# Optimization experiments

Hardware: AMD Instinct MI355X
Metric: run time of the kernel (lower is better)

The kernel has to match this reference:

```python
import jax, jax.numpy as jnp
import numpy as np

B, N, D, H = 8, 1024, 768, 12
HD = D // H  # head_dim = 64


def setup_inputs() -> dict:
    key = jax.random.key(0)
    ks = jax.random.split(key, 7)
    s = 1.0 / np.sqrt(D)  # xavier-ish scale for weights
    return {
        "x1": jax.random.normal(ks[0], (B, N, D), dtype=jnp.float32),
        "x2": jax.random.normal(ks[1], (B, N, D), dtype=jnp.float32),
        "Wq": jax.random.normal(ks[2], (D, D), dtype=jnp.float32) * s,
        "Wk": jax.random.normal(ks[3], (D, D), dtype=jnp.float32) * s,
        "Wv": jax.random.normal(ks[4], (D, D), dtype=jnp.float32) * s,
        "Wo": jax.random.normal(ks[5], (D, D), dtype=jnp.float32) * s,
        "bo": jnp.zeros((D,), dtype=jnp.float32),
    }


def _heads(x):
    # (B, N, D) -> (B, H, N, HD)
    return x.reshape(B, -1, H, HD).transpose(0, 2, 1, 3)


def reference(x1, x2, Wq, Wk, Wv, Wo, bo):
    scale = 1.0 / jnp.sqrt(jnp.asarray(HD, x1.dtype))
    q1 = _heads(x1 @ Wq.T)               # (B,H,N,HD)
    k1 = _heads(x1 @ Wk.T)
    v1 = _heads(x1 @ Wv.T)
    k2 = _heads(x2 @ Wk.T)
    v2 = _heads(x2 @ Wv.T)
    kc = jnp.concatenate([k1, k2], axis=2)   # (B,H,2N,HD)
    vc = jnp.concatenate([v1, v2], axis=2)
    attn = jnp.einsum('bhnd,bhmd->bhnm', q1, kc) * scale  # (B,H,N,2N)
    attn = jax.nn.softmax(attn, axis=-1)
    out = jnp.einsum('bhnm,bhmd->bhnd', attn, vc)          # (B,H,N,HD)
    out = out.transpose(0, 2, 1, 3).reshape(B, N, D)
    return out @ Wo.T + bo
```

## Files before the change

### kernel.cpp

```cpp
#include <hip/hip_runtime.h>


typedef __bf16 bf16x8 __attribute__((ext_vector_type(8)));
typedef float  f32x4  __attribute__((ext_vector_type(4)));
typedef unsigned int u32x4 __attribute__((ext_vector_type(4)));
typedef short  s16x4  __attribute__((ext_vector_type(4)));

__device__ __forceinline__ unsigned short bf16bits(float f) {
    return __builtin_bit_cast(unsigned short, (__bf16)f);
}
__device__ __forceinline__ unsigned pk2(float a, float b) {
    return (unsigned)bf16bits(a) | ((unsigned)bf16bits(b) << 16);
}
__device__ __forceinline__ bf16x8 asbf(u32x4 v) {
    return __builtin_bit_cast(bf16x8, v);
}
__device__ __forceinline__ float fexp2(float x) {
#if __has_builtin(__builtin_amdgcn_exp2f)
    return __builtin_amdgcn_exp2f(x);
#else
    return exp2f(x);
#endif
}
__device__ __forceinline__ float frcp(float x) {
#if __has_builtin(__builtin_amdgcn_rcpf)
    return __builtin_amdgcn_rcpf(x);
#else
    return 1.0f / x;
#endif
}

#define MFMA32(a, b, c) __builtin_amdgcn_mfma_f32_16x16x32_bf16((a), (b), (c), 0, 0, 0)

__global__ __launch_bounds__(256) void convert_all(
    const float* __restrict__ x1, const float* __restrict__ x2,
    const float* __restrict__ Wq, const float* __restrict__ Wk,
    const float* __restrict__ Wv, const float* __restrict__ Wo,
    unsigned short* __restrict__ x1b, unsigned short* __restrict__ x2b,
    unsigned short* __restrict__ Wcat, unsigned short* __restrict__ Wob)
{
    const float* src; unsigned short* dst; int n4;
    switch (blockIdx.y) {
        case 0:  src = x1; dst = x1b;            n4 = 1572864; break;
        case 1:  src = x2; dst = x2b;            n4 = 1572864; break;
        case 2:  src = Wq; dst = Wcat;           n4 = 147456;  break;
        case 3:  src = Wk; dst = Wcat +  589824; n4 = 147456;  break;
        case 4:  src = Wv; dst = Wcat + 1179648; n4 = 147456;  break;
        default: src = Wo; dst = Wob;            n4 = 147456;  break;
    }
    int i = blockIdx.x * 256 + threadIdx.x;
    if (i >= n4) return;
    float4 v = ((const float4*)src)[i];
    unsigned* o32 = (unsigned*)(dst + (size_t)i * 4);
    o32[0] = pk2(v.x, v.y);
    o32[1] = pk2(v.z, v.w);
}

template<int MODE>
__global__ __launch_bounds__(256) void gemm_qkv(
    const unsigned short* __restrict__ A1, const unsigned short* __restrict__ A2,
    const unsigned short* __restrict__ Wcat,
    unsigned short* __restrict__ dQ, unsigned short* __restrict__ dK,
    unsigned short* __restrict__ dV)
{
    __shared__ u32x4 smA[2048];
    __shared__ u32x4 smB[2048];

    const int tid  = threadIdx.x;
    const int lane = tid & 63;
    const int l15  = lane & 15;
    const int g    = lane >> 4;
    const int wid  = tid >> 6;
    const int rb   = blockIdx.x;
    const int jb   = blockIdx.y;
    const int wr   = (wid >> 1) * 64;
    const int wc   = (wid & 1) * 64;

    const bool br2 = (jb >= 18);
    const unsigned short* A  = br2 ? A2 : A1;
    const unsigned short* Bw = br2 ? (Wcat + 589824) : Wcat;
    const int jcol = br2 ? (jb - 18) : jb;

    f32x4 acc[4][4] = {};

#define GSTAGE(KT, BO)                                                               \
    {                                                                                \
        int kt_ = (KT);                                                              \
        _Pragma("unroll")                                                            \
        for (int c_ = 0; c_ < 4; ++c_) {                                             \
            int i_   = (wid + c_ * 4) * 64 + lane;                                   \
            int row_ = i_ >> 3;                                                      \
            int gs_  = (i_ & 7) ^ (row_ & 7);                                        \
            const unsigned short* sa = A +                                           \
                (size_t)(rb * 128 + row_) * 768 + kt_ * 64 + gs_ * 8;                \
            __builtin_amdgcn_global_load_lds(                                        \
                (const __attribute__((address_space(1))) void*)sa,                   \
                (__attribute__((address_space(3))) void*)(smA + (BO) + (wid + c_ * 4) * 64), \
                16, 0, 0);                                                           \
            const unsigned short* sb = Bw +                                          \
                (size_t)(jcol * 128 + row_) * 768 + kt_ * 64 + gs_ * 8;              \
            __builtin_amdgcn_global_load_lds(                                        \
                (const __attribute__((address_space(1))) void*)sb,                   \
                (__attribute__((address_space(3))) void*)(smB + (BO) + (wid + c_ * 4) * 64), \
                16, 0, 0);                                                           \
        }                                                                            \
    }

    GSTAGE(0, 0)

    for (int kt = 0; kt < 12; ++kt) {
        __builtin_amdgcn_s_barrier();
        if (kt < 11) {
            GSTAGE(kt + 1, ((kt + 1) & 1) << 10)
            asm volatile("s_waitcnt vmcnt(8)" ::: "memory");
        } else {
            asm volatile("s_waitcnt vmcnt(0)" ::: "memory");
        }
        __builtin_amdgcn_s_barrier();
        __builtin_amdgcn_sched_barrier(0);

        const u32x4* bA = smA + ((kt & 1) << 10);
        const u32x4* bB = smB + ((kt & 1) << 10);

#pragma unroll
        for (int kk = 0; kk < 2; ++kk) {
            bf16x8 af[4], bfr[4];
#pragma unroll
            for (int m = 0; m < 4; ++m) {
                int row = wr + m * 16 + l15;
                af[m] = asbf(bA[row * 8 + ((kk * 4 + g) ^ (row & 7))]);
            }
#pragma unroll
            for (int n = 0; n < 4; ++n) {
                int row = wc + n * 16 + l15;
                bfr[n] = asbf(bB[row * 8 + ((kk * 4 + g) ^ (row & 7))]);
            }
#pragma unroll
            for (int m = 0; m < 4; ++m)
#pragma unroll
                for (int n = 0; n < 4; ++n)
                    acc[m][n] = MFMA32(af[m], bfr[n], acc[m][n]);
        }
    }
#undef GSTAGE

    const int rloc = wr + g * 4;
    const int cloc = wc + l15;
    const int seg  = jcol / 6;
#pragma unroll
    for (int m = 0; m < 4; ++m) {
#pragma unroll
        for (int n = 0; n < 4; ++n) {
            int r0 = rb * 128 + rloc + m * 16;
            int c  = jcol * 128 + cloc + n * 16;
            int b = r0 >> 10, nn = r0 & 1023;
            int cl = c - seg * 768;
            int h = cl >> 6, hd = cl & 63;
            int segq = br2 ? seg + 3 : seg;
            if (segq == 0) {
#pragma unroll
                for (int reg = 0; reg < 4; ++reg)
                    dQ[((size_t)(b * 12 + h) * 1024 + nn + reg) * 64 + hd] =
                        bf16bits(acc[m][n][reg] * 0.18033688f);
            } else if (segq == 1 || segq == 3) {
                size_t koff = (segq == 3) ? 1024 : 0;
#pragma unroll
                for (int reg = 0; reg < 4; ++reg)
                    dK[((size_t)(b * 12 + h) * 2048 + koff + nn + reg) * 64 + hd] =
                        bf16bits(acc[m][n][reg]);
            } else {
                size_t koff = (segq == 4) ? 1024 : 0;
                uint2 w;
                w.x = pk2(acc[m][n][0], acc[m][n][1]);
                w.y = pk2(acc[m][n][2], acc[m][n][3]);
                *(uint2*)(dV + ((size_t)(b * 12 + h) * 64 + hd) * 2048 +
                          koff + nn) = w;
            }
        }
    }
}

__global__ __launch_bounds__(256) void gemm_out(
    const unsigned short* __restrict__ A, const unsigned short* __restrict__ Bw,
    float* __restrict__ dO, const float* __restrict__ bias)
{
    __shared__ u32x4 smA[2048];
    __shared__ u32x4 smB[2048];

    const int tid  = threadIdx.x;
    const int lane = tid & 63;
    const int l15  = lane & 15;
    const int g    = lane >> 4;
    const int wid  = tid >> 6;
    const int rb   = blockIdx.x;
    const int jb   = blockIdx.y;
    const int wr   = (wid >> 1) * 64;
    const int wc   = (wid & 1) * 64;

    f32x4 acc[4][4] = {};

#define GSTAGE(KT, BO)                                                               \
    {                                                                                \
        int kt_ = (KT);                                                              \
        _Pragma("unroll")                                                            \
        for (int c_ = 0; c_ < 4; ++c_) {                                             \
            int i_   = (wid + c_ * 4) * 64 + lane;                                   \
            int row_ = i_ >> 3;                                                      \
            int gs_  = (i_ & 7) ^ (row_ & 7);                                        \
            const unsigned short* sa = A +                                           \
                (size_t)(rb * 128 + row_) * 768 + kt_ * 64 + gs_ * 8;                \
            __builtin_amdgcn_global_load_lds(                                        \
                (const __attribute__((address_space(1))) void*)sa,                   \
                (__attribute__((address_space(3))) void*)(smA + (BO) + (wid + c_ * 4) * 64), \
                16, 0, 0);                                                           \
            const unsigned short* sb = Bw +                                          \
                (size_t)(jb * 128 + row_) * 768 + kt_ * 64 + gs_ * 8;                \
            __builtin_amdgcn_global_load_lds(                                        \
                (const __attribute__((address_space(1))) void*)sb,                   \
                (__attribute__((address_space(3))) void*)(smB + (BO) + (wid + c_ * 4) * 64), \
                16, 0, 0);                                                           \
        }                                                                            \
    }

    GSTAGE(0, 0)

    for (int kt = 0; kt < 12; ++kt) {
        __builtin_amdgcn_s_barrier();
        if (kt < 11) {
            GSTAGE(kt + 1, ((kt + 1) & 1) << 10)
            asm volatile("s_waitcnt vmcnt(8)" ::: "memory");
        } else {
            asm volatile("s_waitcnt vmcnt(0)" ::: "memory");
        }
        __builtin_amdgcn_s_barrier();
        __builtin_amdgcn_sched_barrier(0);

        const u32x4* bA = smA + ((kt & 1) << 10);
        const u32x4* bB = smB + ((kt & 1) << 10);

#pragma unroll
        for (int kk = 0; kk < 2; ++kk) {
            bf16x8 af[4], bfr[4];
#pragma unroll
            for (int m = 0; m < 4; ++m) {
                int row = wr + m * 16 + l15;
                af[m] = asbf(bA[row * 8 + ((kk * 4 + g) ^ (row & 7))]);
            }
#pragma unroll
            for (int n = 0; n < 4; ++n) {
                int row = wc + n * 16 + l15;
                bfr[n] = asbf(bB[row * 8 + ((kk * 4 + g) ^ (row & 7))]);
            }
#pragma unroll
            for (int m = 0; m < 4; ++m)
#pragma unroll
                for (int n = 0; n < 4; ++n)
                    acc[m][n] = MFMA32(af[m], bfr[n], acc[m][n]);
        }
    }
#undef GSTAGE

    const int rloc = wr + g * 4;
    const int cloc = wc + l15;
#pragma unroll
    for (int m = 0; m < 4; ++m)
#pragma unroll
        for (int n = 0; n < 4; ++n) {
            int r0 = rb * 128 + rloc + m * 16;
            int c  = jb * 128 + cloc + n * 16;
#pragma unroll
            for (int reg = 0; reg < 4; ++reg)
                dO[(size_t)(r0 + reg) * 768 + c] = acc[m][n][reg] + bias[c];
        }
}

__global__ __launch_bounds__(256, 2) void attn_k(
    const unsigned short* __restrict__ Q, const unsigned short* __restrict__ K,
    const unsigned short* __restrict__ Vt, unsigned short* __restrict__ AO)
{
    __shared__ u32x4 sK[1536];
    __shared__ u32x4 sV[1536];

    const int tid  = threadIdx.x;
    const int lane = tid & 63;
    const int g    = lane >> 4;
    const int l15  = lane & 15;
    const int wid  = tid >> 6;
    const int bh   = blockIdx.x;
    const int q0   = blockIdx.y * 256;

    const unsigned short* Qh = Q  + (size_t)bh * (1024 * 64);
    const unsigned short* Kh = K  + (size_t)bh * (2048 * 64);
    const unsigned short* Vh = Vt + (size_t)bh * (64 * 2048);

    bf16x8 qf[4][2];
#pragma unroll
    for (int m = 0; m < 4; ++m)
#pragma unroll
        for (int kk = 0; kk < 2; ++kk)
            qf[m][kk] = *(const bf16x8*)(Qh +
                (size_t)(q0 + wid * 64 + m * 16 + l15) * 64 + kk * 32 + g * 8);

    f32x4 o[4][4] = {};
    float lr[4] = {0.f, 0.f, 0.f, 0.f};

#define STAGE_TILE(T, DOFF)                                                          \
    {                                                                                \
        int t_ = (T);                                                                \
        _Pragma("unroll")                                                            \
        for (int c_ = 0; c_ < 2; ++c_) {                                             \
            int i_   = (wid + c_ * 4) * 64 + lane;                                   \
            int row_ = i_ >> 3;                                                      \
            int gsK_ = (i_ & 7) ^ ((row_ & 3) | ((row_ >> 1) & 4));                  \
            int gsV_ = (i_ & 7) ^ (row_ & 7);                                        \
            const unsigned short* srcK_ = Kh + ((size_t)t_ * 64 + row_) * 64 + gsK_ * 8; \
            __builtin_amdgcn_global_load_lds(                                        \
                (const __attribute__((address_space(1))) void*)srcK_,               \
                (__attribute__((address_space(3))) void*)(sK + (DOFF) + (wid + c_ * 4) * 64), \
                16, 0, 0);                                                           \
            const unsigned short* srcV_ = Vh + (size_t)row_ * 2048 + t_ * 64 + gsV_ * 8; \
            __builtin_amdgcn_global_load_lds(                                        \
                (const __attribute__((address_space(1))) void*)srcV_,               \
                (__attribute__((address_space(3))) void*)(sV + (DOFF) + (wid + c_ * 4) * 64), \
                16, 0, 0);                                                           \
        }                                                                            \
    }

    STAGE_TILE(0, 0)
    STAGE_TILE(1, 512)

    for (int t = 0; t < 32; ++t) {
        if (t < 31) { asm volatile("s_waitcnt vmcnt(4)" ::: "memory"); }
        else        { asm volatile("s_waitcnt vmcnt(0)" ::: "memory"); }
        __builtin_amdgcn_s_barrier();
        if (t < 30) {
            STAGE_TILE(t + 2, ((t + 2) % 3) * 512)
        }
        __builtin_amdgcn_sched_barrier(0);

        const u32x4* sKb = sK + (t % 3) * 512;
        const u32x4* sVb = sV + (t % 3) * 512;

        f32x4 s[4][4] = {};
        __builtin_amdgcn_s_setprio(1);
#pragma unroll
        for (int kk = 0; kk < 2; ++kk) {
            bf16x8 kf[4];
#pragma unroll
            for (int n = 0; n < 4; ++n) {
                int rowp = ((n & 1) << 5) + ((l15 >> 2) << 3) +
                           (((n >> 1) & 1) << 2) + (l15 & 3);
                kf[n] = asbf(sKb[rowp * 8 + ((kk * 4 + g) ^ (l15 & 7))]);
            }
#pragma unroll
            for (int n = 0; n < 4; ++n)
#pragma unroll
                for (int m = 0; m < 4; ++m)
                    s[n][m] = MFMA32(kf[n], qf[m][kk], s[n][m]);
        }
        __builtin_amdgcn_s_setprio(0);

        s16x4 p16[4][4];
#pragma unroll
        for (int m = 0; m < 4; ++m) {
            float sum = 0.f;
#pragma unroll
            for (int n = 0; n < 4; ++n) {
                float p0 = fexp2(s[n][m][0]), p1 = fexp2(s[n][m][1]);
                float p2 = fexp2(s[n][m][2]), p3 = fexp2(s[n][m][3]);
                sum += (p0 + p1) + (p2 + p3);
                p16[n][m] = (s16x4){ (short)bf16bits(p0), (short)bf16bits(p1),
                                     (short)bf16bits(p2), (short)bf16bits(p3) };
            }
            lr[m] += sum;
        }

        __builtin_amdgcn_s_setprio(1);
#pragma unroll
        for (int kk = 0; kk < 2; ++kk) {
            bf16x8 pf[4];
#pragma unroll
            for (int m = 0; m < 4; ++m)
                pf[m] = __builtin_bit_cast(bf16x8,
                    __builtin_shufflevector(p16[kk][m], p16[kk + 2][m],
                                            0, 1, 2, 3, 4, 5, 6, 7));
#pragma unroll
            for (int v = 0; v < 4; ++v) {
                int row = v * 16 + l15;
                bf16x8 vf = asbf(sVb[row * 8 + ((kk * 4 + g) ^ (row & 7))]);
#pragma unroll
                for (int m = 0; m < 4; ++m)
                    o[v][m] = MFMA32(vf, pf[m], o[v][m]);
            }
        }
        __builtin_amdgcn_s_setprio(0);
    }

    const int b = bh / 12, h = bh % 12;
#pragma unroll
    for (int m = 0; m < 4; ++m) {
        float l = lr[m];
        l += __shfl_xor(l, 16); l += __shfl_xor(l, 32);
        float rl = frcp(l);
        int q = q0 + wid * 64 + m * 16 + l15;
        unsigned short* dst = AO + (size_t)(b * 1024 + q) * 768 + h * 64 + g * 4;
#pragma unroll
        for (int v = 0; v < 4; ++v) {
            uint2 w;
            w.x = pk2(o[v][m][0] * rl, o[v][m][1] * rl);
            w.y = pk2(o[v][m][2] * rl, o[v][m][3] * rl);
            *(uint2*)(dst + v * 16) = w;
        }
    }
#undef STAGE_TILE
}

extern "C" void kernel_launch(void* const* d_in, const int* in_sizes, int n_in,
                              void* d_out, int out_size, void* d_ws, size_t ws_size,
                              hipStream_t stream)
{
    const float* x1 = (const float*)d_in[0];
    const float* x2 = (const float*)d_in[1];
    const float* Wq = (const float*)d_in[2];
    const float* Wk = (const float*)d_in[3];
    const float* Wv = (const float*)d_in[4];
    const float* Wo = (const float*)d_in[5];
    const float* bo = (const float*)d_in[6];

    unsigned short* Wcat = (unsigned short*)d_ws;
    unsigned short* Wob  = Wcat + 1769472;
    unsigned short* x1b  = Wob  + 589824;
    unsigned short* x2b  = x1b  + 6291456;
    unsigned short* Qb   = x2b  + 6291456;
    unsigned short* Kc   = Qb   + 6291456;
    unsigned short* Vt   = Kc   + 12582912;
    unsigned short* AO   = x1b;

    convert_all<<<dim3(6144, 6), 256, 0, stream>>>(x1, x2, Wq, Wk, Wv, Wo,
                                                   x1b, x2b, Wcat, Wob);

    gemm_qkv<0><<<dim3(64, 30), 256, 0, stream>>>(x1b, x2b, Wcat, Qb, Kc, Vt);

    attn_k<<<dim3(96, 4), 256, 0, stream>>>(Qb, Kc, Vt, AO);

    gemm_out<<<dim3(64, 6), 256, 0, stream>>>(AO, Wob, (float*)d_out, bo);
}
```

Before: 168.7 us.

## Halve attention query tile, load V directly to registers, raise occupancy

The attention kernel now handles 128 queries per block instead of 256 (32 per wave), doubling the grid to 768 blocks and raising launch bounds to 3 blocks per CU. V tiles are no longer staged through LDS; each wave reads its V fragments straight from global memory into registers, while K keeps the triple-buffered LDS path. This cuts LDS use and register pressure to allow more resident waves. In exchange, K/V traffic per query doubles and the uncoalesced per-wave global V loads may add latency that the reduced per-wave work has less room to hide.

Measured after the change: 197.8 us. 17.3% more time.

```diff
diff --git a/kernel.cpp b/kernel.cpp
--- a/kernel.cpp
+++ b/kernel.cpp
@@ -274,12 +274,11 @@
         }
 }
 
-__global__ __launch_bounds__(256, 2) void attn_k(
+__global__ __launch_bounds__(256, 3) void attn_k(
     const unsigned short* __restrict__ Q, const unsigned short* __restrict__ K,
     const unsigned short* __restrict__ Vt, unsigned short* __restrict__ AO)
 {
     __shared__ u32x4 sK[1536];
-    __shared__ u32x4 sV[1536];
 
     const int tid  = threadIdx.x;
     const int lane = tid & 63;
@@ -287,24 +286,26 @@
     const int l15  = lane & 15;
     const int wid  = tid >> 6;
     const int bh   = blockIdx.x;
-    const int q0   = blockIdx.y * 256;
+    const int q0   = blockIdx.y * 128;
 
     const unsigned short* Qh = Q  + (size_t)bh * (1024 * 64);
     const unsigned short* Kh = K  + (size_t)bh * (2048 * 64);
     const unsigned short* Vh = Vt + (size_t)bh * (64 * 2048);
 
-    bf16x8 qf[4][2];
-#pragma unroll
-    for (int m = 0; m < 4; ++m)
+    bf16x8 qf[2][2];
+#pragma unroll
+    for (int m = 0; m < 2; ++m)
 #pragma unroll
         for (int kk = 0; kk < 2; ++kk)
             qf[m][kk] = *(const bf16x8*)(Qh +
-                (size_t)(q0 + wid * 64 + m * 16 + l15) * 64 + kk * 32 + g * 8);
-
-    f32x4 o[4][4] = {};
-    float lr[4] = {0.f, 0.f, 0.f, 0.f};
-
-#define STAGE_TILE(T, DOFF)                                                          \
+                (size_t)(q0 + wid * 32 + m * 16 + l15) * 64 + kk * 32 + g * 8);
+
+    const unsigned short* vrow0 = Vh + (size_t)l15 * 2048 + g * 8;
+
+    f32x4 o[4][2] = {};
+    float lr0 = 0.f, lr1 = 0.f;
+
+#define STAGE_K(T, DOFF)                                                             \
     {                                                                                \
         int t_ = (T);                                                                \
         _Pragma("unroll")                                                            \
@@ -312,36 +313,35 @@
             int i_   = (wid + c_ * 4) * 64 + lane;                                   \
             int row_ = i_ >> 3;                                                      \
             int gsK_ = (i_ & 7) ^ ((row_ & 3) | ((row_ >> 1) & 4));                  \
-            int gsV_ = (i_ & 7) ^ (row_ & 7);                                        \
             const unsigned short* srcK_ = Kh + ((size_t)t_ * 64 + row_) * 64 + gsK_ * 8; \
             __builtin_amdgcn_global_load_lds(                                        \
                 (const __attribute__((address_space(1))) void*)srcK_,               \
                 (__attribute__((address_space(3))) void*)(sK + (DOFF) + (wid + c_ * 4) * 64), \
                 16, 0, 0);                                                           \
-            const unsigned short* srcV_ = Vh + (size_t)row_ * 2048 + t_ * 64 + gsV_ * 8; \
-            __builtin_amdgcn_global_load_lds(                                        \
-                (const __attribute__((address_space(1))) void*)srcV_,               \
-                (__attribute__((address_space(3))) void*)(sV + (DOFF) + (wid + c_ * 4) * 64), \
-                16, 0, 0);                                                           \
         }                                                                            \
     }
 
-    STAGE_TILE(0, 0)
-    STAGE_TILE(1, 512)
+    STAGE_K(0, 0)
+    STAGE_K(1, 512)
+    asm volatile("s_waitcnt vmcnt(2)" ::: "memory");
 
     for (int t = 0; t < 32; ++t) {
-        if (t < 31) { asm volatile("s_waitcnt vmcnt(4)" ::: "memory"); }
-        else        { asm volatile("s_waitcnt vmcnt(0)" ::: "memory"); }
         __builtin_amdgcn_s_barrier();
-        if (t < 30) {
-            STAGE_TILE(t + 2, ((t + 2) % 3) * 512)
-        }
+
+        bf16x8 vf[4][2];
+#pragma unroll
+        for (int v = 0; v < 4; ++v) {
+            const unsigned short* vr = vrow0 + (size_t)v * (16 * 2048) + t * 64;
+#pragma unroll
+            for (int kk = 0; kk < 2; ++kk)
+                vf[v][kk] = *(const bf16x8*)(vr + kk * 32);
+        }
+        if (t < 30) STAGE_K(t + 2, ((t + 2) % 3) * 512)
         __builtin_amdgcn_sched_barrier(0);
 
         const u32x4* sKb = sK + (t % 3) * 512;
-        const u32x4* sVb = sV + (t % 3) * 512;
-
-        f32x4 s[4][4] = {};
+
+        f32x4 s[4][2] = {};
         __builtin_amdgcn_s_setprio(1);
 #pragma unroll
         for (int kk = 0; kk < 2; ++kk) {
@@ -355,54 +355,58 @@
 #pragma unroll
             for (int n = 0; n < 4; ++n)
 #pragma unroll
-                for (int m = 0; m < 4; ++m)
+                for (int m = 0; m < 2; ++m)
                     s[n][m] = MFMA32(kf[n], qf[m][kk], s[n][m]);
         }
         __builtin_amdgcn_s_setprio(0);
 
-        s16x4 p16[4][4];
-#pragma unroll
-        for (int m = 0; m < 4; ++m) {
-            float sum = 0.f;
-#pragma unroll
-            for (int n = 0; n < 4; ++n) {
-                float p0 = fexp2(s[n][m][0]), p1 = fexp2(s[n][m][1]);
-                float p2 = fexp2(s[n][m][2]), p3 = fexp2(s[n][m][3]);
-                sum += (p0 + p1) + (p2 + p3);
-                p16[n][m] = (s16x4){ (short)bf16bits(p0), (short)bf16bits(p1),
-                                     (short)bf16bits(p2), (short)bf16bits(p3) };
-            }
-            lr[m] += sum;
-        }
+        float sum0 = 0.f, sum1 = 0.f;
+        s16x4 p16[4][2];
+#pragma unroll
+        for (int n = 0; n < 4; ++n) {
+            float p00 = fexp2(s[n][0][0]), p01 = fexp2(s[n][0][1]);
+            float p02 = fexp2(s[n][0][2]), p03 = fexp2(s[n][0][3]);
+            float p10 = fexp2(s[n][1][0]), p11 = fexp2(s[n][1][1]);
+            float p12 = fexp2(s[n][1][2]), p13 = fexp2(s[n][1][3]);
+            sum0 += (p00 + p01) + (p02 + p03);
+            sum1 += (p10 + p11) + (p12 + p13);
+            uint2 w0, w1;
+            w0.x = pk2(p00, p01); w0.y = pk2(p02, p03);
+            w1.x = pk2(p10, p11); w1.y = pk2(p12, p13);
+            p16[n][0] = __builtin_bit_cast(s16x4, w0);
+            p16[n][1] = __builtin_bit_cast(s16x4, w1);
+        }
+        lr0 += sum0; lr1 += sum1;
+
+        if (t < 30) { asm volatile("s_waitcnt vmcnt(2)" ::: "memory"); }
+        else        { asm volatile("s_waitcnt vmcnt(0)" ::: "memory"); }
 
         __builtin_amdgcn_s_setprio(1);
 #pragma unroll
         for (int kk = 0; kk < 2; ++kk) {
-            bf16x8 pf[4];
-#pragma unroll
-            for (int m = 0; m < 4; ++m)
+            bf16x8 pf[2];
+#pragma unroll
+            for (int m = 0; m < 2; ++m)
                 pf[m] = __builtin_bit_cast(bf16x8,
                     __builtin_shufflevector(p16[kk][m], p16[kk + 2][m],
                                             0, 1, 2, 3, 4, 5, 6, 7));
 #pragma unroll
-            for (int v = 0; v < 4; ++v) {
-                int row = v * 16 + l15;
-                bf16x8 vf = asbf(sVb[row * 8 + ((kk * 4 + g) ^ (row & 7))]);
-#pragma unroll
-                for (int m = 0; m < 4; ++m)
-                    o[v][m] = MFMA32(vf, pf[m], o[v][m]);
-            }
+            for (int v = 0; v < 4; ++v)
+#pragma unroll
+                for (int m = 0; m < 2; ++m)
+                    o[v][m] = MFMA32(vf[v][kk], pf[m], o[v][m]);
         }
         __builtin_amdgcn_s_setprio(0);
     }
 
+    lr0 += __shfl_xor(lr0, 16); lr0 += __shfl_xor(lr0, 32);
+    lr1 += __shfl_xor(lr1, 16); lr1 += __shfl_xor(lr1, 32);
     const int b = bh / 12, h = bh % 12;
-#pragma unroll
-    for (int m = 0; m < 4; ++m) {
-        float l = lr[m];
-        l += __shfl_xor(l, 16); l += __shfl_xor(l, 32);
-        float rl = frcp(l);
-        int q = q0 + wid * 64 + m * 16 + l15;
+    float rl0 = frcp(lr0), rl1 = frcp(lr1);
+#pragma unroll
+    for (int m = 0; m < 2; ++m) {
+        float rl = m ? rl1 : rl0;
+        int q = q0 + wid * 32 + m * 16 + l15;
         unsigned short* dst = AO + (size_t)(b * 1024 + q) * 768 + h * 64 + g * 4;
 #pragma unroll
         for (int v = 0; v < 4; ++v) {
@@ -412,7 +416,7 @@
             *(uint2*)(dst + v * 16) = w;
         }
     }
-#undef STAGE_TILE
+#undef STAGE_K
 }
 
 extern "C" void kernel_launch(void* const* d_in, const int* in_sizes, int n_in,
@@ -441,7 +445,7 @@
 
     gemm_qkv<0><<<dim3(64, 30), 256, 0, stream>>>(x1b, x2b, Wcat, Qb, Kc, Vt);
 
-    attn_k<<<dim3(96, 4), 256, 0, stream>>>(Qb, Kc, Vt, AO);
+    attn_k<<<dim3(96, 8), 256, 0, stream>>>(Qb, Kc, Vt, AO);
 
     gemm_out<<<dim3(64, 6), 256, 0, stream>>>(AO, Wob, (float*)d_out, bo);
 }
```

## Split attention KV tiles across wave pairs and reduce partial outputs via LDS

Applied to the files above, without the earlier changes.

The attention kernel now gives each block 128 queries instead of 256. Each pair of waves splits the 64-key tile in half: each wave covers 32 keys for its 64 queries. Partial outputs and row sums are combined through LDS at the end, and the grid doubles to 768 blocks with launch bounds raised to 3 blocks per CU. The goal is better occupancy and load balance on the 256-CU device, since 384 blocks underfill it. The cost is that K/V tiles are staged into LDS twice as often per query, plus an extra LDS reduction and syncs at the end.

Result: faster. 158.6 us (-6.0%).

```diff
diff --git a/kernel.cpp b/kernel.cpp
--- a/kernel.cpp
+++ b/kernel.cpp
@@ -274,7 +274,7 @@
         }
 }
 
-__global__ __launch_bounds__(256, 2) void attn_k(
+__global__ __launch_bounds__(256, 3) void attn_k(
     const unsigned short* __restrict__ Q, const unsigned short* __restrict__ K,
     const unsigned short* __restrict__ Vt, unsigned short* __restrict__ AO)
 {
@@ -286,8 +286,10 @@
     const int g    = lane >> 4;
     const int l15  = lane & 15;
     const int wid  = tid >> 6;
+    const int qh   = wid & 1;
+    const int kvh  = wid >> 1;
     const int bh   = blockIdx.x;
-    const int q0   = blockIdx.y * 256;
+    const int q0   = blockIdx.y * 128;
 
     const unsigned short* Qh = Q  + (size_t)bh * (1024 * 64);
     const unsigned short* Kh = K  + (size_t)bh * (2048 * 64);
@@ -299,7 +301,7 @@
 #pragma unroll
         for (int kk = 0; kk < 2; ++kk)
             qf[m][kk] = *(const bf16x8*)(Qh +
-                (size_t)(q0 + wid * 64 + m * 16 + l15) * 64 + kk * 32 + g * 8);
+                (size_t)(q0 + qh * 64 + m * 16 + l15) * 64 + kk * 32 + g * 8);
 
     f32x4 o[4][4] = {};
     float lr[4] = {0.f, 0.f, 0.f, 0.f};
@@ -341,75 +343,98 @@
         const u32x4* sKb = sK + (t % 3) * 512;
         const u32x4* sVb = sV + (t % 3) * 512;
 
-        f32x4 s[4][4] = {};
+        f32x4 s[2][4] = {};
         __builtin_amdgcn_s_setprio(1);
 #pragma unroll
         for (int kk = 0; kk < 2; ++kk) {
-            bf16x8 kf[4];
-#pragma unroll
-            for (int n = 0; n < 4; ++n) {
-                int rowp = ((n & 1) << 5) + ((l15 >> 2) << 3) +
-                           (((n >> 1) & 1) << 2) + (l15 & 3);
-                kf[n] = asbf(sKb[rowp * 8 + ((kk * 4 + g) ^ (l15 & 7))]);
-            }
-#pragma unroll
-            for (int n = 0; n < 4; ++n)
+            bf16x8 kf[2];
+#pragma unroll
+            for (int j = 0; j < 2; ++j) {
+                int rowp = (kvh << 5) + ((l15 >> 2) << 3) + (j << 2) + (l15 & 3);
+                kf[j] = asbf(sKb[rowp * 8 + ((kk * 4 + g) ^ (l15 & 7))]);
+            }
+#pragma unroll
+            for (int j = 0; j < 2; ++j)
 #pragma unroll
                 for (int m = 0; m < 4; ++m)
-                    s[n][m] = MFMA32(kf[n], qf[m][kk], s[n][m]);
+                    s[j][m] = MFMA32(kf[j], qf[m][kk], s[j][m]);
         }
         __builtin_amdgcn_s_setprio(0);
 
-        s16x4 p16[4][4];
+        s16x4 p16[2][4];
 #pragma unroll
         for (int m = 0; m < 4; ++m) {
-            float sum = 0.f;
-#pragma unroll
-            for (int n = 0; n < 4; ++n) {
-                float p0 = fexp2(s[n][m][0]), p1 = fexp2(s[n][m][1]);
-                float p2 = fexp2(s[n][m][2]), p3 = fexp2(s[n][m][3]);
-                sum += (p0 + p1) + (p2 + p3);
-                p16[n][m] = (s16x4){ (short)bf16bits(p0), (short)bf16bits(p1),
-                                     (short)bf16bits(p2), (short)bf16bits(p3) };
-            }
-            lr[m] += sum;
+            float p0 = fexp2(s[0][m][0]), p1 = fexp2(s[0][m][1]);
+            float p2 = fexp2(s[0][m][2]), p3 = fexp2(s[0][m][3]);
+            float p4 = fexp2(s[1][m][0]), p5 = fexp2(s[1][m][1]);
+            float p6 = fexp2(s[1][m][2]), p7 = fexp2(s[1][m][3]);
+            lr[m] += (p0 + p1) + (p2 + p3) + (p4 + p5) + (p6 + p7);
+            p16[0][m] = (s16x4){ (short)bf16bits(p0), (short)bf16bits(p1),
+                                 (short)bf16bits(p2), (short)bf16bits(p3) };
+            p16[1][m] = (s16x4){ (short)bf16bits(p4), (short)bf16bits(p5),
+                                 (short)bf16bits(p6), (short)bf16bits(p7) };
         }
 
         __builtin_amdgcn_s_setprio(1);
-#pragma unroll
-        for (int kk = 0; kk < 2; ++kk) {
-            bf16x8 pf[4];
+        bf16x8 pf[4];
+#pragma unroll
+        for (int m = 0; m < 4; ++m)
+            pf[m] = __builtin_bit_cast(bf16x8,
+                __builtin_shufflevector(p16[0][m], p16[1][m],
+                                        0, 1, 2, 3, 4, 5, 6, 7));
+#pragma unroll
+        for (int v = 0; v < 4; ++v) {
+            int row = v * 16 + l15;
+            bf16x8 vf = asbf(sVb[row * 8 + ((kvh * 4 + g) ^ (row & 7))]);
 #pragma unroll
             for (int m = 0; m < 4; ++m)
-                pf[m] = __builtin_bit_cast(bf16x8,
-                    __builtin_shufflevector(p16[kk][m], p16[kk + 2][m],
-                                            0, 1, 2, 3, 4, 5, 6, 7));
+                o[v][m] = MFMA32(vf, pf[m], o[v][m]);
+        }
+        __builtin_amdgcn_s_setprio(0);
+    }
+
+#pragma unroll
+    for (int m = 0; m < 4; ++m) {
+        lr[m] += __shfl_xor(lr[m], 16);
+        lr[m] += __shfl_xor(lr[m], 32);
+    }
+    __syncthreads();
+
+    float* oK   = (float*)sK;
+    float* oVf  = (float*)sV;
+    float* obuf = qh ? oVf : oK;
+    float* lbuf = oVf + 64 * 72;
+
+    if (kvh == 1) {
+#pragma unroll
+        for (int m = 0; m < 4; ++m)
+#pragma unroll
+            for (int v = 0; v < 4; ++v)
+                *(f32x4*)&obuf[(m * 16 + l15) * 72 + v * 16 + g * 4] = o[v][m];
+        if (lane < 16) {
+#pragma unroll
+            for (int m = 0; m < 4; ++m)
+                lbuf[qh * 64 + m * 16 + l15] = lr[m];
+        }
+    }
+    __syncthreads();
+
+    if (kvh == 0) {
+        const int b = bh / 12, h = bh % 12;
+#pragma unroll
+        for (int m = 0; m < 4; ++m) {
+            float lt = lr[m] + lbuf[qh * 64 + m * 16 + l15];
+            float rl = frcp(lt);
+            int q = q0 + qh * 64 + m * 16 + l15;
+            unsigned short* dst = AO + (size_t)(b * 1024 + q) * 768 + h * 64 + g * 4;
 #pragma unroll
             for (int v = 0; v < 4; ++v) {
-                int row = v * 16 + l15;
-                bf16x8 vf = asbf(sVb[row * 8 + ((kk * 4 + g) ^ (row & 7))]);
-#pragma unroll
-                for (int m = 0; m < 4; ++m)
-                    o[v][m] = MFMA32(vf, pf[m], o[v][m]);
-            }
-        }
-        __builtin_amdgcn_s_setprio(0);
-    }
-
-    const int b = bh / 12, h = bh % 12;
-#pragma unroll
-    for (int m = 0; m < 4; ++m) {
-        float l = lr[m];
-        l += __shfl_xor(l, 16); l += __shfl_xor(l, 32);
-        float rl = frcp(l);
-        int q = q0 + wid * 64 + m * 16 + l15;
-        unsigned short* dst = AO + (size_t)(b * 1024 + q) * 768 + h * 64 + g * 4;
-#pragma unroll
-        for (int v = 0; v < 4; ++v) {
-            uint2 w;
-            w.x = pk2(o[v][m][0] * rl, o[v][m][1] * rl);
-            w.y = pk2(o[v][m][2] * rl, o[v][m][3] * rl);
-            *(uint2*)(dst + v * 16) = w;
+                f32x4 add = *(const f32x4*)&obuf[(m * 16 + l15) * 72 + v * 16 + g * 4];
+                uint2 w;
+                w.x = pk2((o[v][m][0] + add[0]) * rl, (o[v][m][1] + add[1]) * rl);
+                w.y = pk2((o[v][m][2] + add[2]) * rl, (o[v][m][3] + add[3]) * rl);
+                *(uint2*)(dst + v * 16) = w;
+            }
         }
     }
 #undef STAGE_TILE
@@ -441,7 +466,7 @@
 
     gemm_qkv<0><<<dim3(64, 30), 256, 0, stream>>>(x1b, x2b, Wcat, Qb, Kc, Vt);
 
-    attn_k<<<dim3(96, 4), 256, 0, stream>>>(Qb, Kc, Vt, AO);
+    attn_k<<<dim3(96, 8), 256, 0, stream>>>(Qb, Kc, Vt, AO);
 
     gemm_out<<<dim3(64, 6), 256, 0, stream>>>(AO, Wob, (float*)d_out, bo);
 }
```
